# Kernel optimization log

Measured on AMD Instinct MI355X. Metric: run time of the kernel, lower is better.

## Reference

```python
import jax, jax.numpy as jnp
import numpy as np

B, S, D = 2, 4096, 512
H = 8
HD = D // H  # 64


def setup_inputs() -> dict:
    key = jax.random.key(0)
    ks = jax.random.split(key, 9)
    sc = 1.0 / np.sqrt(D)
    inp = {
        "x": jax.random.normal(ks[0], (B, S, D), dtype=jnp.float32),
        "W_q": jax.random.normal(ks[1], (D, D), dtype=jnp.float32) * sc,
        "b_q": jax.random.normal(ks[2], (D,), dtype=jnp.float32) * 0.01,
        "W_k": jax.random.normal(ks[3], (D, D), dtype=jnp.float32) * sc,
        "b_k": jax.random.normal(ks[4], (D,), dtype=jnp.float32) * 0.01,
        "W_v": jax.random.normal(ks[5], (D, D), dtype=jnp.float32) * sc,
        "b_v": jax.random.normal(ks[6], (D,), dtype=jnp.float32) * 0.01,
        "W_o": jax.random.normal(ks[7], (D, D), dtype=jnp.float32) * sc,
        "b_o": jax.random.normal(ks[8], (D,), dtype=jnp.float32) * 0.01,
    }
    return inp


def reference(x, W_q, b_q, W_k, b_k, W_v, b_v, W_o, b_o):
    # QKV projections (torch Linear: x @ W.T + b)
    q = x @ W_q.T + b_q  # [B,S,D]
    k = x @ W_k.T + b_k
    v = x @ W_v.T + b_v
    # split heads -> [B,H,S,HD]
    def split(t):
        return t.reshape(B, S, H, HD).transpose(0, 2, 1, 3)
    q, k, v = split(q), split(k), split(v)
    scale = 1.0 / jnp.sqrt(jnp.float32(HD))
    scores = jnp.einsum("bhsd,bhtd->bhst", q, k) * scale  # [B,H,S,S]
    weights = jax.nn.softmax(scores, axis=-1)
    attn = jnp.einsum("bhst,bhtd->bhsd", weights, v)  # [B,H,S,HD]
    attn = attn.transpose(0, 2, 1, 3).reshape(B, S, D)
    return attn @ W_o.T + b_o
```

## Files before the change

### kernel.cpp

```cpp
#include <hip/hip_runtime.h>
#include <hip/hip_bf16.h>
#include <stdint.h>


typedef __attribute__((ext_vector_type(8))) short short8;
typedef __attribute__((ext_vector_type(4))) short sv4;
typedef __attribute__((ext_vector_type(4))) float floatx4;

#define MFMA(a, b, c) __builtin_amdgcn_mfma_f32_16x16x32_bf16((a), (b), (c), 0, 0, 0)

typedef __attribute__((address_space(1))) const void* gas_t;
typedef __attribute__((address_space(3))) void* las_t;
#define GLDS16(g, l) __builtin_amdgcn_global_load_lds((gas_t)(g), (las_t)(l), 16, 0, 0)

#define SM_SHIFT 13.0f

__device__ __forceinline__ float fexp2(float x) {
#if __has_builtin(__builtin_amdgcn_exp2f)
    return __builtin_amdgcn_exp2f(x);
#else
    float r;
    asm("v_exp_f32 %0, %1" : "=v"(r) : "v"(x));
    return r;
#endif
}

__device__ __forceinline__ short f2bf(float f) {
    union { float f; uint32_t u; } c; c.f = f;
    uint32_t u = c.u;
    u += 0x7fffu + ((u >> 16) & 1u);
    return (short)(u >> 16);
}
__device__ __forceinline__ float bf2f(short s) {
    union { float f; uint32_t u; } c; c.u = ((uint32_t)(uint16_t)s) << 16;
    return c.f;
}
__device__ __forceinline__ int pack2(float a, float b) {
    return (int)(uint16_t)f2bf(a) | ((int)(uint16_t)f2bf(b) << 16);
}
__device__ __forceinline__ int pack2rn(float a, float b) {
#if __has_builtin(__builtin_amdgcn_cvt_pk_bf16_f32)
    auto r = __builtin_amdgcn_cvt_pk_bf16_f32(a, b);
    int out; __builtin_memcpy(&out, &r, 4);
    return out;
#else
    int r;
    asm("v_cvt_pk_bf16_f32 %0, %1, %2" : "=v"(r) : "v"(a), "v"(b));
    return r;
#endif
}

__global__ void cvt_all(const float* __restrict__ x,
                        const float* __restrict__ wq, const float* __restrict__ wk,
                        const float* __restrict__ wv, const float* __restrict__ wo,
                        short* __restrict__ xb, short* __restrict__ wqb,
                        short* __restrict__ wkb, short* __restrict__ wvb,
                        short* __restrict__ wohi, short* __restrict__ wolo)
{
    int bid = blockIdx.x;
    if (bid < 2048) {
        int i = (bid * 256 + threadIdx.x) * 8;
        floatx4 v0 = *(const floatx4*)(x + i);
        floatx4 v1 = *(const floatx4*)(x + i + 4);
        short8 o;
        #pragma unroll
        for (int j = 0; j < 4; ++j) { o[j] = f2bf(v0[j]); o[4 + j] = f2bf(v1[j]); }
        *(short8*)(xb + i) = o;
    } else if (bid < 2432) {
        int idx = (bid - 2048) * 256 + threadIdx.x;
        int which = idx >> 15;
        int i = (idx & 32767) * 8;
        const float* src = which == 0 ? wq : which == 1 ? wk : wv;
        short* dst = which == 0 ? wqb : which == 1 ? wkb : wvb;
        floatx4 v0 = *(const floatx4*)(src + i);
        floatx4 v1 = *(const floatx4*)(src + i + 4);
        short8 o;
        #pragma unroll
        for (int j = 0; j < 4; ++j) { o[j] = f2bf(v0[j]); o[4 + j] = f2bf(v1[j]); }
        *(short8*)(dst + i) = o;
    } else {
        int i = ((bid - 2432) * 256 + threadIdx.x) * 8;
        floatx4 v0 = *(const floatx4*)(wo + i);
        floatx4 v1 = *(const floatx4*)(wo + i + 4);
        short8 h, l;
        #pragma unroll
        for (int j = 0; j < 4; ++j) {
            short hh = f2bf(v0[j]); h[j] = hh; l[j] = f2bf(v0[j] - bf2f(hh));
            short hh1 = f2bf(v1[j]); h[4 + j] = hh1; l[4 + j] = f2bf(v1[j] - bf2f(hh1));
        }
        *(short8*)(wohi + i) = h;
        *(short8*)(wolo + i) = l;
    }
}

__global__ __launch_bounds__(256) void qkv_gemm(
    const short* __restrict__ Xb,
    const short* __restrict__ Wq, const short* __restrict__ Wk, const short* __restrict__ Wv,
    const float* __restrict__ bq, const float* __restrict__ bk, const float* __restrict__ bv,
    short* __restrict__ Qo, short* __restrict__ Ko, short* __restrict__ VTo)
{
    __shared__ short SMEM[16384];
    #define ASH(bf) (SMEM + (bf) * 4096)
    #define BSH(bf) (SMEM + 8192 + (bf) * 4096)
    const int lane = threadIdx.x & 63, wave = threadIdx.x >> 6;
    const int col = lane & 15, quad = lane >> 4;
    const int wm = wave & 1, wn = wave >> 1;
    const int m0 = blockIdx.x * 128;
    const int by = blockIdx.y;
    const int which = by >> 2;
    const int n0 = (by & 3) * 128;
    const short* W = which == 0 ? Wq : which == 1 ? Wk : Wv;
    const float* bias = which == 0 ? bq : which == 1 ? bk : bv;
    const float oscale = which == 0 ? 0.1803368801111204f : 1.0f;

    const int rl = lane >> 2, pch = lane & 3;
    const int lch = pch ^ (rl & 3) ^ ((rl >> 2) & 3);
    const int seg = wave * 2;
    const short* ag0 = Xb + (size_t)(m0 + seg * 16 + rl) * 512 + lch * 8;
    const short* ag1 = ag0 + (size_t)16 * 512;
    const short* bg0 = W + (size_t)(n0 + seg * 16 + rl) * 512 + lch * 8;
    const short* bg1 = bg0 + (size_t)16 * 512;

    floatx4 acc[4][4] = {};

    GLDS16(ag0, ASH(0) + seg * 512);
    GLDS16(ag1, ASH(0) + (seg + 1) * 512);
    GLDS16(bg0, BSH(0) + seg * 512);
    GLDS16(bg1, BSH(0) + (seg + 1) * 512);
    __syncthreads();

    for (int t = 0; t < 16; ++t) {
        const int cur = t & 1;
        if (t < 15) {
            const int kb = (t + 1) * 32;
            GLDS16(ag0 + kb, ASH(cur ^ 1) + seg * 512);
            GLDS16(ag1 + kb, ASH(cur ^ 1) + (seg + 1) * 512);
            GLDS16(bg0 + kb, BSH(cur ^ 1) + seg * 512);
            GLDS16(bg1 + kb, BSH(cur ^ 1) + (seg + 1) * 512);
        }
        short8 af[4], bf[4];
        #pragma unroll
        for (int it = 0; it < 4; ++it) {
            const int rA = wm * 64 + it * 16 + col;
            const int pA = quad ^ (rA & 3) ^ ((rA >> 2) & 3);
            af[it] = *(const short8*)(ASH(cur) + rA * 32 + pA * 8);
            const int rB = wn * 64 + it * 16 + col;
            const int pB = quad ^ (rB & 3) ^ ((rB >> 2) & 3);
            bf[it] = *(const short8*)(BSH(cur) + rB * 32 + pB * 8);
        }
        #pragma unroll
        for (int i = 0; i < 4; ++i)
            #pragma unroll
            for (int j = 0; j < 4; ++j)
                acc[i][j] = MFMA(af[i], bf[j], acc[i][j]);
        __syncthreads();
    }

    if (which < 2) {
        #pragma unroll
        for (int i = 0; i < 4; ++i)
            #pragma unroll
            for (int j = 0; j < 4; ++j)
                #pragma unroll
                for (int r = 0; r < 4; ++r) {
                    int m = m0 + wm * 64 + i * 16 + quad * 4 + r;
                    int n = n0 + wn * 64 + j * 16 + col;
                    float v = (acc[i][j][r] + bias[n]) * oscale;
                    int b = m >> 12, s = m & 4095;
                    int h = n >> 6, hd = n & 63;
                    int bh = b * 8 + h;
                    short bv16 = f2bf(v);
                    if (which == 0) Qo[((size_t)bh * 4096 + s) * 64 + hd] = bv16;
                    else            Ko[((size_t)bh * 4096 + s) * 64 + hd] = bv16;
                }
    } else {
        short* tb = SMEM + wave * 4096;
        #pragma unroll
        for (int n2 = 0; n2 < 2; ++n2) {
            #pragma unroll
            for (int jj = 0; jj < 2; ++jj) {
                const int j = n2 * 2 + jj;
                const int n_rel = jj * 16 + col;
                const float bv_ = bias[n0 + wn * 64 + j * 16 + col];
                #pragma unroll
                for (int i = 0; i < 4; ++i) {
                    const int m_rel = i * 16 + quad * 4;
                    *(int*)(tb + n_rel * 72 + m_rel) =
                        pack2(acc[i][j][0] + bv_, acc[i][j][1] + bv_);
                    *(int*)(tb + n_rel * 72 + m_rel + 2) =
                        pack2(acc[i][j][2] + bv_, acc[i][j][3] + bv_);
                }
            }
            asm volatile("s_waitcnt lgkmcnt(0)" ::: "memory");
            const int n_rel = lane & 31, half = lane >> 5;
            const int n = n0 + wn * 64 + n2 * 32 + n_rel;
            const int h = n >> 6, hd = n & 63;
            const int bh = (m0 >> 12) * 8 + h;
            const int s0 = (m0 & 4095) + wm * 64 + half * 32;
            const short* src = tb + n_rel * 72 + half * 32;
            short* dst = VTo + ((size_t)bh * 64 + hd) * 4096 + s0;
            #pragma unroll
            for (int c = 0; c < 4; ++c)
                *(int4*)(dst + c * 8) = *(const int4*)(src + c * 8);
        }
    }
    #undef ASH
    #undef BSH
}

__device__ __forceinline__ void softmax_pk(
    const floatx4* sa, floatx4& lacc, short8 ones8, short8* pb)
{
    #pragma unroll
    for (int c = 0; c < 2; ++c) {
        union { int i[4]; short8 s; } u;
        #pragma unroll
        for (int h = 0; h < 2; ++h) {
            float p0 = fexp2(sa[2 * c + h][0]);
            float p1 = fexp2(sa[2 * c + h][1]);
            float p2 = fexp2(sa[2 * c + h][2]);
            float p3 = fexp2(sa[2 * c + h][3]);
            u.i[2 * h]     = pack2rn(p0, p1);
            u.i[2 * h + 1] = pack2rn(p2, p3);
        }
        pb[c] = u.s;
        lacc = MFMA(ones8, u.s, lacc);
    }
}

__global__ __launch_bounds__(512, 4) void flash_attn(
    const short* __restrict__ Q, const short* __restrict__ Kk,
    const short* __restrict__ VT,
    short* __restrict__ Ahi, short* __restrict__ Alo)
{
    __shared__ float SMEMf[16384];
    short* SMEM = (short*)SMEMf;
    const int lane = threadIdx.x & 63, wave = threadIdx.x >> 6;
    const int col = lane & 15, quad = lane >> 4;
    const int id = blockIdx.x;
    const int bh = (id & 7) * 2 + (id >> 8);
    const int bx = (id >> 3) & 31;
    const int b = bh >> 3, h = bh & 7;
    const int qw = wave & 3, kz = wave >> 2;
    const int q0 = bx * 128 + qw * 32;
    const int kbeg = kz * 2048;
    const size_t base = (size_t)bh * 4096 * 64;
    const size_t vbase = (size_t)bh * 64 * 4096;

    const short* qptr = Q + base + (size_t)(q0 + col) * 64 + quad * 8;
    short8 qA0 = *(const short8*)(qptr);
    short8 qA1 = *(const short8*)(qptr + 32);
    short8 qB0 = *(const short8*)(qptr + 16 * 64);
    short8 qB1 = *(const short8*)(qptr + 16 * 64 + 32);

    const int rloc = lane >> 3, pch = lane & 7;
    const int lch = pch ^ rloc;
    const short* kst0 = Kk + base + (size_t)(kbeg + qw * 16 + rloc) * 64 + lch * 8;
    const short* kst1 = kst0 + (size_t)8 * 64;
    const short* vst0 = VT + vbase + (size_t)(qw * 16 + rloc) * 4096 + kbeg + lch * 8;
    const short* vst1 = vst0 + (size_t)8 * 4096;

    floatx4 oA[4] = {}, oB[4] = {};
    floatx4 laccA = {0.f, 0.f, 0.f, 0.f}, laccB = {0.f, 0.f, 0.f, 0.f};
    const floatx4 mshift = {-SM_SHIFT, -SM_SHIFT, -SM_SHIFT, -SM_SHIFT};
    short8 ones8;
    #pragma unroll
    for (int j = 0; j < 8; ++j) ones8[j] = (short)0x3F80;

    const int sw = col & 7;
    const int co0 = (quad ^ sw) * 8;
    const int co1 = ((quad + 4) ^ sw) * 8;
    int voff[4];
    #pragma unroll
    for (int nt = 0; nt < 4; ++nt)
        voff[nt] = ((2 * nt + (quad >> 1)) ^ sw) * 8 + (quad & 1) * 4;

    const short* kb0 = SMEM + kz * 8192 + col * 64 + co0;
    const short* kb1 = SMEM + kz * 8192 + col * 64 + co1;
    const short* vb0 = SMEM + 16384 + kz * 8192 + col * 64 + voff[0];
    const short* vb1 = SMEM + 16384 + kz * 8192 + col * 64 + voff[1];
    const short* vb2 = SMEM + 16384 + kz * 8192 + col * 64 + voff[2];
    const short* vb3 = SMEM + 16384 + kz * 8192 + col * 64 + voff[3];
    short* const klds0 = SMEM + kz * 8192 + qw * 1024;
    short* const klds1 = klds0 + 4096;
    short* const vlds0 = SMEM + 16384 + kz * 8192 + qw * 1024;
    short* const vlds1 = vlds0 + 4096;

    {
        GLDS16(kst0, klds0);
        GLDS16(kst1, klds0 + 8 * 64);
        GLDS16(vst0, vlds0);
        GLDS16(vst1, vlds0 + 8 * 64);
    }
    __syncthreads();

#define FA_BODY(CUR, KO2, PF)                                                  \
    {                                                                          \
        if (PF) {                                                              \
            GLDS16(kst0 + (size_t)(KO2) * 64, (CUR) ? klds0 : klds1);          \
            GLDS16(kst1 + (size_t)(KO2) * 64, ((CUR) ? klds0 : klds1) + 512);  \
            GLDS16(vst0 + (KO2), (CUR) ? vlds0 : vlds1);                       \
            GLDS16(vst1 + (KO2), ((CUR) ? vlds0 : vlds1) + 512);               \
        }                                                                      \
        floatx4 saA[4], saB[4];                                                \
        __builtin_amdgcn_s_setprio(1);                                         \
        _Pragma("unroll")                                                      \
        for (int nt = 0; nt < 4; ++nt) {                                       \
            short8 k0 = *(const short8*)(kb0 + (CUR) * 4096 + nt * 1024);      \
            short8 k1 = *(const short8*)(kb1 + (CUR) * 4096 + nt * 1024);      \
            floatx4 z = MFMA(k0, qA0, mshift);                                 \
            saA[nt] = MFMA(k1, qA1, z);                                        \
            floatx4 z2 = MFMA(k0, qB0, mshift);                                \
            saB[nt] = MFMA(k1, qB1, z2);                                       \
        }                                                                      \
        __builtin_amdgcn_s_setprio(0);                                         \
        short8 pbA[2], pbB[2];                                                 \
        softmax_pk(saA, laccA, ones8, pbA);                                    \
        softmax_pk(saB, laccB, ones8, pbB);                                    \
        __builtin_amdgcn_s_setprio(1);                                         \
        _Pragma("unroll")                                                      \
        for (int mt = 0; mt < 4; ++mt) {                                       \
            union { sv4 h[2]; short8 s; } u0, u1;                              \
            u0.h[0] = *(const sv4*)(vb0 + (CUR) * 4096 + mt * 1024);           \
            u0.h[1] = *(const sv4*)(vb1 + (CUR) * 4096 + mt * 1024);           \
            u1.h[0] = *(const sv4*)(vb2 + (CUR) * 4096 + mt * 1024);           \
            u1.h[1] = *(const sv4*)(vb3 + (CUR) * 4096 + mt * 1024);           \
            oA[mt] = MFMA(u0.s, pbA[0], oA[mt]);                               \
            oB[mt] = MFMA(u0.s, pbB[0], oB[mt]);                               \
            oA[mt] = MFMA(u1.s, pbA[1], oA[mt]);                               \
            oB[mt] = MFMA(u1.s, pbB[1], oB[mt]);                               \
        }                                                                      \
        __builtin_amdgcn_s_setprio(0);                                         \
        __syncthreads();                                                       \
    }

    int ko2 = 64;
    for (int t2 = 0; t2 < 15; ++t2) {
        FA_BODY(0, ko2, 1); ko2 += 64;
        FA_BODY(1, ko2, 1); ko2 += 64;
    }
    FA_BODY(0, ko2, 1);
    FA_BODY(1, 0, 0);
#undef FA_BODY

    float lA = laccA[0], lB = laccB[0];

    float* Osh = SMEMf;
    float* Msh = SMEMf + 8704;
    if (kz == 1) {
        #pragma unroll
        for (int mt = 0; mt < 4; ++mt) {
            *(floatx4*)&Osh[(qw * 2 + 0) * 1088 + col * 68 + mt * 16 + quad * 4] = oA[mt];
            *(floatx4*)&Osh[(qw * 2 + 1) * 1088 + col * 68 + mt * 16 + quad * 4] = oB[mt];
        }
        if (quad == 0) {
            Msh[qw * 32 + col] = lA;
            Msh[qw * 32 + col + 16] = lB;
        }
    }
    __syncthreads();
    if (kz == 0) {
        float linvA = 1.0f / (lA + Msh[qw * 32 + col]);
        float linvB = 1.0f / (lB + Msh[qw * 32 + col + 16]);
        size_t rowA = (size_t)(b * 4096 + q0 + col) * 512 + h * 64;
        size_t rowB = rowA + (size_t)16 * 512;
        #pragma unroll
        for (int mt = 0; mt < 4; ++mt) {
            floatx4 o2A = *(const floatx4*)&Osh[(qw * 2 + 0) * 1088 + col * 68 + mt * 16 + quad * 4];
            floatx4 o2B = *(const floatx4*)&Osh[(qw * 2 + 1) * 1088 + col * 68 + mt * 16 + quad * 4];
            float w0 = (oA[mt][0] + o2A[0]) * linvA;
            float w1 = (oA[mt][1] + o2A[1]) * linvA;
            float w2 = (oA[mt][2] + o2A[2]) * linvA;
            float w3 = (oA[mt][3] + o2A[3]) * linvA;
            int2 hi, lo;
            hi.x = pack2(w0, w1); hi.y = pack2(w2, w3);
            lo.x = pack2(w0 - bf2f(f2bf(w0)), w1 - bf2f(f2bf(w1)));
            lo.y = pack2(w2 - bf2f(f2bf(w2)), w3 - bf2f(f2bf(w3)));
            *(int2*)(Ahi + rowA + mt * 16 + quad * 4) = hi;
            *(int2*)(Alo + rowA + mt * 16 + quad * 4) = lo;
            w0 = (oB[mt][0] + o2B[0]) * linvB;
            w1 = (oB[mt][1] + o2B[1]) * linvB;
            w2 = (oB[mt][2] + o2B[2]) * linvB;
            w3 = (oB[mt][3] + o2B[3]) * linvB;
            hi.x = pack2(w0, w1); hi.y = pack2(w2, w3);
            lo.x = pack2(w0 - bf2f(f2bf(w0)), w1 - bf2f(f2bf(w1)));
            lo.y = pack2(w2 - bf2f(f2bf(w2)), w3 - bf2f(f2bf(w3)));
            *(int2*)(Ahi + rowB + mt * 16 + quad * 4) = hi;
            *(int2*)(Alo + rowB + mt * 16 + quad * 4) = lo;
        }
    }
}

__global__ __launch_bounds__(256) void out_gemm(
    const short* __restrict__ Ahi, const short* __restrict__ Alo,
    const short* __restrict__ Whi, const short* __restrict__ Wlo,
    const float* __restrict__ bo, float* __restrict__ Out)
{
    __shared__ short SMEM[24576];
    #define AHS(bf) (SMEM + (bf) * 4096)
    #define ALS(bf) (SMEM + 8192 + (bf) * 4096)
    #define BHS(bf) (SMEM + 16384 + (bf) * 2048)
    #define BLS(bf) (SMEM + 20480 + (bf) * 2048)
    const int lane = threadIdx.x & 63, wave = threadIdx.x >> 6;
    const int col = lane & 15, quad = lane >> 4;
    const int wm = wave & 1, wn = wave >> 1;
    const int m0 = blockIdx.x * 128;
    const int n0 = blockIdx.y * 64;

    const int rl = lane >> 2, pch = lane & 3;
    const int lch = pch ^ (rl & 3) ^ ((rl >> 2) & 3);
    const int seg = wave * 2;
    const short* ah0 = Ahi + (size_t)(m0 + seg * 16 + rl) * 512 + lch * 8;
    const short* ah1 = ah0 + (size_t)16 * 512;
    const short* al0 = Alo + (size_t)(m0 + seg * 16 + rl) * 512 + lch * 8;
    const short* al1 = al0 + (size_t)16 * 512;
    const short* bh0 = Whi + (size_t)(n0 + wave * 16 + rl) * 512 + lch * 8;
    const short* bl0 = Wlo + (size_t)(n0 + wave * 16 + rl) * 512 + lch * 8;

    floatx4 acc[4][2] = {};

    GLDS16(ah0, AHS(0) + seg * 512);
    GLDS16(ah1, AHS(0) + (seg + 1) * 512);
    GLDS16(al0, ALS(0) + seg * 512);
    GLDS16(al1, ALS(0) + (seg + 1) * 512);
    GLDS16(bh0, BHS(0) + wave * 512);
    GLDS16(bl0, BLS(0) + wave * 512);
    __syncthreads();

    for (int t = 0; t < 16; ++t) {
        const int cur = t & 1;
        if (t < 15) {
            const int kb = (t + 1) * 32;
            GLDS16(ah0 + kb, AHS(cur ^ 1) + seg * 512);
            GLDS16(ah1 + kb, AHS(cur ^ 1) + (seg + 1) * 512);
            GLDS16(al0 + kb, ALS(cur ^ 1) + seg * 512);
            GLDS16(al1 + kb, ALS(cur ^ 1) + (seg + 1) * 512);
            GLDS16(bh0 + kb, BHS(cur ^ 1) + wave * 512);
            GLDS16(bl0 + kb, BLS(cur ^ 1) + wave * 512);
        }
        short8 ahf[4], alf[4], bhf[2], blf[2];
        #pragma unroll
        for (int it = 0; it < 4; ++it) {
            const int rA = wm * 64 + it * 16 + col;
            const int pA = quad ^ (rA & 3) ^ ((rA >> 2) & 3);
            ahf[it] = *(const short8*)(AHS(cur) + rA * 32 + pA * 8);
            alf[it] = *(const short8*)(ALS(cur) + rA * 32 + pA * 8);
        }
        #pragma unroll
        for (int jt = 0; jt < 2; ++jt) {
            const int rB = wn * 32 + jt * 16 + col;
            const int pB = quad ^ (rB & 3) ^ ((rB >> 2) & 3);
            bhf[jt] = *(const short8*)(BHS(cur) + rB * 32 + pB * 8);
            blf[jt] = *(const short8*)(BLS(cur) + rB * 32 + pB * 8);
        }
        #pragma unroll
        for (int i = 0; i < 4; ++i)
            #pragma unroll
            for (int j = 0; j < 2; ++j) {
                acc[i][j] = MFMA(ahf[i], bhf[j], acc[i][j]);
                acc[i][j] = MFMA(ahf[i], blf[j], acc[i][j]);
                acc[i][j] = MFMA(alf[i], bhf[j], acc[i][j]);
            }
        __syncthreads();
    }

    #pragma unroll
    for (int i = 0; i < 4; ++i)
        #pragma unroll
        for (int j = 0; j < 2; ++j)
            #pragma unroll
            for (int r = 0; r < 4; ++r) {
                int m = m0 + wm * 64 + i * 16 + quad * 4 + r;
                int n = n0 + wn * 32 + j * 16 + col;
                Out[(size_t)m * 512 + n] = acc[i][j][r] + bo[n];
            }
    #undef AHS
    #undef ALS
    #undef BHS
    #undef BLS
}

extern "C" void kernel_launch(void* const* d_in, const int* in_sizes, int n_in,
                              void* d_out, int out_size, void* d_ws, size_t ws_size,
                              hipStream_t stream) {
    (void)in_sizes; (void)n_in; (void)out_size; (void)ws_size;
    const float* x   = (const float*)d_in[0];
    const float* W_q = (const float*)d_in[1];
    const float* b_q = (const float*)d_in[2];
    const float* W_k = (const float*)d_in[3];
    const float* b_k = (const float*)d_in[4];
    const float* W_v = (const float*)d_in[5];
    const float* b_v = (const float*)d_in[6];
    const float* W_o = (const float*)d_in[7];
    const float* b_o = (const float*)d_in[8];
    float* out = (float*)d_out;
    char* ws = (char*)d_ws;

    short* Xb   = (short*)(ws + 0);
    short* Wqb  = (short*)(ws + 8388608);
    short* Wkb  = (short*)(ws + 8912896);
    short* Wvb  = (short*)(ws + 9437184);
    short* Wohi = (short*)(ws + 9961472);
    short* Wolo = (short*)(ws + 10485760);
    short* Qb   = (short*)(ws + 11010048);
    short* Kb   = (short*)(ws + 19398656);
    short* VTb  = (short*)(ws + 27787264);
    short* Ahi  = (short*)(ws + 36175872);
    short* Alo  = (short*)(ws + 44564480);

    cvt_all<<<dim3(2560), dim3(256), 0, stream>>>(x, W_q, W_k, W_v, W_o,
                                                  Xb, Wqb, Wkb, Wvb, Wohi, Wolo);
    qkv_gemm<<<dim3(64, 12), dim3(256), 0, stream>>>(Xb, Wqb, Wkb, Wvb, b_q, b_k, b_v, Qb, Kb, VTb);
    flash_attn<<<dim3(512), dim3(512), 0, stream>>>(Qb, Kb, VTb, Ahi, Alo);
    out_gemm<<<dim3(64, 8), dim3(256), 0, stream>>>(Ahi, Alo, Wohi, Wolo, b_o, out);
}
```

Baseline: 196.3 us.

## Double queries per wave in flash attention to reuse K/V fragments across four tiles

```diff
diff --git a/kernel.cpp b/kernel.cpp
--- a/kernel.cpp
+++ b/kernel.cpp
@@ -200,35 +200,19 @@
             const short* src = tb + n_rel * 72 + half * 32;
             short* dst = VTo + ((size_t)bh * 64 + hd) * 4096 + s0;
             #pragma unroll
-            for (int c = 0; c < 4; ++c)
-                *(int4*)(dst + c * 8) = *(const int4*)(src + c * 8);
+            for (int qq = 0; qq < 4; ++qq) {
+                union { sv4 hh[2]; int4 v; } u;
+                u.hh[0] = *(const sv4*)(src + 4 * qq);
+                u.hh[1] = *(const sv4*)(src + 16 + 4 * qq);
+                *(int4*)(dst + qq * 8) = u.v;
+            }
         }
     }
     #undef ASH
     #undef BSH
 }
 
-__device__ __forceinline__ void softmax_pk(
-    const floatx4* sa, floatx4& lacc, short8 ones8, short8* pb)
-{
-    #pragma unroll
-    for (int c = 0; c < 2; ++c) {
-        union { int i[4]; short8 s; } u;
-        #pragma unroll
-        for (int h = 0; h < 2; ++h) {
-            float p0 = fexp2(sa[2 * c + h][0]);
-            float p1 = fexp2(sa[2 * c + h][1]);
-            float p2 = fexp2(sa[2 * c + h][2]);
-            float p3 = fexp2(sa[2 * c + h][3]);
-            u.i[2 * h]     = pack2rn(p0, p1);
-            u.i[2 * h + 1] = pack2rn(p2, p3);
-        }
-        pb[c] = u.s;
-        lacc = MFMA(ones8, u.s, lacc);
-    }
-}
-
-__global__ __launch_bounds__(512, 4) void flash_attn(
+__global__ __launch_bounds__(512, 2) void flash_attn(
     const short* __restrict__ Q, const short* __restrict__ Kk,
     const short* __restrict__ VT,
     short* __restrict__ Ahi, short* __restrict__ Alo)
@@ -238,20 +222,22 @@
     const int lane = threadIdx.x & 63, wave = threadIdx.x >> 6;
     const int col = lane & 15, quad = lane >> 4;
     const int id = blockIdx.x;
-    const int bh = (id & 7) * 2 + (id >> 8);
-    const int bx = (id >> 3) & 31;
+    const int bh = id & 15;
+    const int bx = id >> 4;
     const int b = bh >> 3, h = bh & 7;
     const int qw = wave & 3, kz = wave >> 2;
-    const int q0 = bx * 128 + qw * 32;
+    const int q0 = bx * 256 + qw * 64;
     const int kbeg = kz * 2048;
     const size_t base = (size_t)bh * 4096 * 64;
     const size_t vbase = (size_t)bh * 64 * 4096;
 
-    const short* qptr = Q + base + (size_t)(q0 + col) * 64 + quad * 8;
-    short8 qA0 = *(const short8*)(qptr);
-    short8 qA1 = *(const short8*)(qptr + 32);
-    short8 qB0 = *(const short8*)(qptr + 16 * 64);
-    short8 qB1 = *(const short8*)(qptr + 16 * 64 + 32);
+    short8 qf0[4], qf1[4];
+    #pragma unroll
+    for (int qt = 0; qt < 4; ++qt) {
+        const short* qp = Q + base + (size_t)(q0 + qt * 16 + col) * 64 + quad * 8;
+        qf0[qt] = *(const short8*)(qp);
+        qf1[qt] = *(const short8*)(qp + 32);
+    }
 
     const int rloc = lane >> 3, pch = lane & 7;
     const int lch = pch ^ rloc;
@@ -260,8 +246,8 @@
     const short* vst0 = VT + vbase + (size_t)(qw * 16 + rloc) * 4096 + kbeg + lch * 8;
     const short* vst1 = vst0 + (size_t)8 * 4096;
 
-    floatx4 oA[4] = {}, oB[4] = {};
-    floatx4 laccA = {0.f, 0.f, 0.f, 0.f}, laccB = {0.f, 0.f, 0.f, 0.f};
+    floatx4 o[4][4] = {};
+    floatx4 lacc[4] = {};
     const floatx4 mshift = {-SM_SHIFT, -SM_SHIFT, -SM_SHIFT, -SM_SHIFT};
     short8 ones8;
     #pragma unroll
@@ -270,28 +256,19 @@
     const int sw = col & 7;
     const int co0 = (quad ^ sw) * 8;
     const int co1 = ((quad + 4) ^ sw) * 8;
-    int voff[4];
-    #pragma unroll
-    for (int nt = 0; nt < 4; ++nt)
-        voff[nt] = ((2 * nt + (quad >> 1)) ^ sw) * 8 + (quad & 1) * 4;
-
     const short* kb0 = SMEM + kz * 8192 + col * 64 + co0;
     const short* kb1 = SMEM + kz * 8192 + col * 64 + co1;
-    const short* vb0 = SMEM + 16384 + kz * 8192 + col * 64 + voff[0];
-    const short* vb1 = SMEM + 16384 + kz * 8192 + col * 64 + voff[1];
-    const short* vb2 = SMEM + 16384 + kz * 8192 + col * 64 + voff[2];
-    const short* vb3 = SMEM + 16384 + kz * 8192 + col * 64 + voff[3];
+    const short* vb0 = SMEM + 16384 + kz * 8192 + col * 64 + co0;
+    const short* vb1 = SMEM + 16384 + kz * 8192 + col * 64 + co1;
     short* const klds0 = SMEM + kz * 8192 + qw * 1024;
     short* const klds1 = klds0 + 4096;
     short* const vlds0 = SMEM + 16384 + kz * 8192 + qw * 1024;
     short* const vlds1 = vlds0 + 4096;
 
-    {
-        GLDS16(kst0, klds0);
-        GLDS16(kst1, klds0 + 8 * 64);
-        GLDS16(vst0, vlds0);
-        GLDS16(vst1, vlds0 + 8 * 64);
-    }
+    GLDS16(kst0, klds0);
+    GLDS16(kst1, klds0 + 512);
+    GLDS16(vst0, vlds0);
+    GLDS16(vst1, vlds0 + 512);
     __syncthreads();
 
 #define FA_BODY(CUR, KO2, PF)                                                  \
@@ -302,35 +279,44 @@
             GLDS16(vst0 + (KO2), (CUR) ? vlds0 : vlds1);                       \
             GLDS16(vst1 + (KO2), ((CUR) ? vlds0 : vlds1) + 512);               \
         }                                                                      \
-        floatx4 saA[4], saB[4];                                                \
-        __builtin_amdgcn_s_setprio(1);                                         \
         _Pragma("unroll")                                                      \
-        for (int nt = 0; nt < 4; ++nt) {                                       \
-            short8 k0 = *(const short8*)(kb0 + (CUR) * 4096 + nt * 1024);      \
-            short8 k1 = *(const short8*)(kb1 + (CUR) * 4096 + nt * 1024);      \
-            floatx4 z = MFMA(k0, qA0, mshift);                                 \
-            saA[nt] = MFMA(k1, qA1, z);                                        \
-            floatx4 z2 = MFMA(k0, qB0, mshift);                                \
-            saB[nt] = MFMA(k1, qB1, z2);                                       \
+        for (int c = 0; c < 2; ++c) {                                          \
+            short8 k0a = *(const short8*)(kb0 + (CUR) * 4096 + (2 * c) * 1024);     \
+            short8 k1a = *(const short8*)(kb1 + (CUR) * 4096 + (2 * c) * 1024);     \
+            short8 k0b = *(const short8*)(kb0 + (CUR) * 4096 + (2 * c + 1) * 1024); \
+            short8 k1b = *(const short8*)(kb1 + (CUR) * 4096 + (2 * c + 1) * 1024); \
+            floatx4 saA[4], saB[4];                                            \
+            __builtin_amdgcn_s_setprio(1);                                     \
+            _Pragma("unroll")                                                  \
+            for (int qt = 0; qt < 4; ++qt) {                                   \
+                floatx4 z = MFMA(k0a, qf0[qt], mshift);                        \
+                saA[qt] = MFMA(k1a, qf1[qt], z);                               \
+                floatx4 z2 = MFMA(k0b, qf0[qt], mshift);                       \
+                saB[qt] = MFMA(k1b, qf1[qt], z2);                              \
+            }                                                                  \
+            __builtin_amdgcn_s_setprio(0);                                     \
+            short8 pb[4];                                                      \
+            _Pragma("unroll")                                                  \
+            for (int qt = 0; qt < 4; ++qt) {                                   \
+                union { int i[4]; short8 s; } u;                               \
+                u.i[0] = pack2rn(fexp2(saA[qt][0]), fexp2(saA[qt][1]));        \
+                u.i[1] = pack2rn(fexp2(saA[qt][2]), fexp2(saA[qt][3]));        \
+                u.i[2] = pack2rn(fexp2(saB[qt][0]), fexp2(saB[qt][1]));        \
+                u.i[3] = pack2rn(fexp2(saB[qt][2]), fexp2(saB[qt][3]));        \
+                pb[qt] = u.s;                                                  \
+                lacc[qt] = MFMA(ones8, u.s, lacc[qt]);                         \
+            }                                                                  \
+            __builtin_amdgcn_s_setprio(1);                                     \
+            _Pragma("unroll")                                                  \
+            for (int mt = 0; mt < 4; ++mt) {                                   \
+                const short8 vv = *(const short8*)(((c) ? vb1 : vb0) + (CUR) * 4096 + mt * 1024); \
+                o[0][mt] = MFMA(vv, pb[0], o[0][mt]);                          \
+                o[1][mt] = MFMA(vv, pb[1], o[1][mt]);                          \
+                o[2][mt] = MFMA(vv, pb[2], o[2][mt]);                          \
+                o[3][mt] = MFMA(vv, pb[3], o[3][mt]);                          \
+            }                                                                  \
+            __builtin_amdgcn_s_setprio(0);                                     \
         }                                                                      \
-        __builtin_amdgcn_s_setprio(0);                                         \
-        short8 pbA[2], pbB[2];                                                 \
-        softmax_pk(saA, laccA, ones8, pbA);                                    \
-        softmax_pk(saB, laccB, ones8, pbB);                                    \
-        __builtin_amdgcn_s_setprio(1);                                         \
-        _Pragma("unroll")                                                      \
-        for (int mt = 0; mt < 4; ++mt) {                                       \
-            union { sv4 h[2]; short8 s; } u0, u1;                              \
-            u0.h[0] = *(const sv4*)(vb0 + (CUR) * 4096 + mt * 1024);           \
-            u0.h[1] = *(const sv4*)(vb1 + (CUR) * 4096 + mt * 1024);           \
-            u1.h[0] = *(const sv4*)(vb2 + (CUR) * 4096 + mt * 1024);           \
-            u1.h[1] = *(const sv4*)(vb3 + (CUR) * 4096 + mt * 1024);           \
-            oA[mt] = MFMA(u0.s, pbA[0], oA[mt]);                               \
-            oB[mt] = MFMA(u0.s, pbB[0], oB[mt]);                               \
-            oA[mt] = MFMA(u1.s, pbA[1], oA[mt]);                               \
-            oB[mt] = MFMA(u1.s, pbB[1], oB[mt]);                               \
-        }                                                                      \
-        __builtin_amdgcn_s_setprio(0);                                         \
         __syncthreads();                                                       \
     }
 
@@ -343,51 +329,54 @@
     FA_BODY(1, 0, 0);
 #undef FA_BODY
 
-    float lA = laccA[0], lB = laccB[0];
-
     float* Osh = SMEMf;
     float* Msh = SMEMf + 8704;
-    if (kz == 1) {
-        #pragma unroll
-        for (int mt = 0; mt < 4; ++mt) {
-            *(floatx4*)&Osh[(qw * 2 + 0) * 1088 + col * 68 + mt * 16 + quad * 4] = oA[mt];
-            *(floatx4*)&Osh[(qw * 2 + 1) * 1088 + col * 68 + mt * 16 + quad * 4] = oB[mt];
-        }
-        if (quad == 0) {
-            Msh[qw * 32 + col] = lA;
-            Msh[qw * 32 + col + 16] = lB;
-        }
-    }
-    __syncthreads();
-    if (kz == 0) {
-        float linvA = 1.0f / (lA + Msh[qw * 32 + col]);
-        float linvB = 1.0f / (lB + Msh[qw * 32 + col + 16]);
-        size_t rowA = (size_t)(b * 4096 + q0 + col) * 512 + h * 64;
-        size_t rowB = rowA + (size_t)16 * 512;
-        #pragma unroll
-        for (int mt = 0; mt < 4; ++mt) {
-            floatx4 o2A = *(const floatx4*)&Osh[(qw * 2 + 0) * 1088 + col * 68 + mt * 16 + quad * 4];
-            floatx4 o2B = *(const floatx4*)&Osh[(qw * 2 + 1) * 1088 + col * 68 + mt * 16 + quad * 4];
-            float w0 = (oA[mt][0] + o2A[0]) * linvA;
-            float w1 = (oA[mt][1] + o2A[1]) * linvA;
-            float w2 = (oA[mt][2] + o2A[2]) * linvA;
-            float w3 = (oA[mt][3] + o2A[3]) * linvA;
-            int2 hi, lo;
-            hi.x = pack2(w0, w1); hi.y = pack2(w2, w3);
-            lo.x = pack2(w0 - bf2f(f2bf(w0)), w1 - bf2f(f2bf(w1)));
-            lo.y = pack2(w2 - bf2f(f2bf(w2)), w3 - bf2f(f2bf(w3)));
-            *(int2*)(Ahi + rowA + mt * 16 + quad * 4) = hi;
-            *(int2*)(Alo + rowA + mt * 16 + quad * 4) = lo;
-            w0 = (oB[mt][0] + o2B[0]) * linvB;
-            w1 = (oB[mt][1] + o2B[1]) * linvB;
-            w2 = (oB[mt][2] + o2B[2]) * linvB;
-            w3 = (oB[mt][3] + o2B[3]) * linvB;
-            hi.x = pack2(w0, w1); hi.y = pack2(w2, w3);
-            lo.x = pack2(w0 - bf2f(f2bf(w0)), w1 - bf2f(f2bf(w1)));
-            lo.y = pack2(w2 - bf2f(f2bf(w2)), w3 - bf2f(f2bf(w3)));
-            *(int2*)(Ahi + rowB + mt * 16 + quad * 4) = hi;
-            *(int2*)(Alo + rowB + mt * 16 + quad * 4) = lo;
-        }
+    #pragma unroll
+    for (int p = 0; p < 2; ++p) {
+        const int ta = 2 * p, tb_ = 2 * p + 1;
+        if (kz == 1) {
+            #pragma unroll
+            for (int mt = 0; mt < 4; ++mt) {
+                *(floatx4*)&Osh[(qw * 2 + 0) * 1088 + col * 68 + mt * 16 + quad * 4] = o[ta][mt];
+                *(floatx4*)&Osh[(qw * 2 + 1) * 1088 + col * 68 + mt * 16 + quad * 4] = o[tb_][mt];
+            }
+            if (quad == 0) {
+                Msh[qw * 32 + col] = lacc[ta][0];
+                Msh[qw * 32 + col + 16] = lacc[tb_][0];
+            }
+        }
+        __syncthreads();
+        if (kz == 0) {
+            float linvA = 1.0f / (lacc[ta][0] + Msh[qw * 32 + col]);
+            float linvB = 1.0f / (lacc[tb_][0] + Msh[qw * 32 + col + 16]);
+            size_t rowA = (size_t)(b * 4096 + q0 + ta * 16 + col) * 512 + h * 64;
+            size_t rowB = rowA + (size_t)16 * 512;
+            #pragma unroll
+            for (int mt = 0; mt < 4; ++mt) {
+                floatx4 o2A = *(const floatx4*)&Osh[(qw * 2 + 0) * 1088 + col * 68 + mt * 16 + quad * 4];
+                floatx4 o2B = *(const floatx4*)&Osh[(qw * 2 + 1) * 1088 + col * 68 + mt * 16 + quad * 4];
+                float w0 = (o[ta][mt][0] + o2A[0]) * linvA;
+                float w1 = (o[ta][mt][1] + o2A[1]) * linvA;
+                float w2 = (o[ta][mt][2] + o2A[2]) * linvA;
+                float w3 = (o[ta][mt][3] + o2A[3]) * linvA;
+                int2 hi, lo;
+                hi.x = pack2(w0, w1); hi.y = pack2(w2, w3);
+                lo.x = pack2(w0 - bf2f(f2bf(w0)), w1 - bf2f(f2bf(w1)));
+                lo.y = pack2(w2 - bf2f(f2bf(w2)), w3 - bf2f(f2bf(w3)));
+                *(int2*)(Ahi + rowA + mt * 16 + quad * 4) = hi;
+                *(int2*)(Alo + rowA + mt * 16 + quad * 4) = lo;
+                w0 = (o[tb_][mt][0] + o2B[0]) * linvB;
+                w1 = (o[tb_][mt][1] + o2B[1]) * linvB;
+                w2 = (o[tb_][mt][2] + o2B[2]) * linvB;
+                w3 = (o[tb_][mt][3] + o2B[3]) * linvB;
+                hi.x = pack2(w0, w1); hi.y = pack2(w2, w3);
+                lo.x = pack2(w0 - bf2f(f2bf(w0)), w1 - bf2f(f2bf(w1)));
+                lo.y = pack2(w2 - bf2f(f2bf(w2)), w3 - bf2f(f2bf(w3)));
+                *(int2*)(Ahi + rowB + mt * 16 + quad * 4) = hi;
+                *(int2*)(Alo + rowB + mt * 16 + quad * 4) = lo;
+            }
+        }
+        __syncthreads();
     }
 }
 
@@ -511,6 +500,6 @@
     cvt_all<<<dim3(2560), dim3(256), 0, stream>>>(x, W_q, W_k, W_v, W_o,
                                                   Xb, Wqb, Wkb, Wvb, Wohi, Wolo);
     qkv_gemm<<<dim3(64, 12), dim3(256), 0, stream>>>(Xb, Wqb, Wkb, Wvb, b_q, b_k, b_v, Qb, Kb, VTb);
-    flash_attn<<<dim3(512), dim3(512), 0, stream>>>(Qb, Kb, VTb, Ahi, Alo);
+    flash_attn<<<dim3(256), dim3(512), 0, stream>>>(Qb, Kb, VTb, Ahi, Alo);
     out_gemm<<<dim3(64, 8), dim3(256), 0, stream>>>(Ahi, Alo, Wohi, Wolo, b_o, out);
 }
```

New measurement: 184.5 us. 6.0% less time.
